# Kernel tuning notes

Hardware: AMD Instinct MI355X
Metric: run time of the kernel (lower is better)

Reference implementation:

```python
import jax, jax.numpy as jnp
import numpy as np

EMB_SCALE = 0.001  # embedding_scale when normalize=False


def setup_inputs() -> dict:
    key = jax.random.key(0)
    k1, k2 = jax.random.split(key)
    N, S, C, V, K = 8, 4096, 2, 128, 512
    x0 = jax.random.normal(k1, (N, S, C, V), dtype=jnp.float32)
    embedding = jax.random.normal(k2, (C, K, V), dtype=jnp.float32) * EMB_SCALE
    return {"x0": x0, "embedding": embedding}


def reference(x0, embedding):
    # normalize=False path: x = x0, embedding used as-is
    N, S, C, V = x0.shape
    K = embedding.shape[1]
    x = x0
    xf = x.reshape(N * S, C, V)  # (B, C, V), B = N*S tokens

    # (the ||x||^2 term is constant over k). Avoids materializing (B, C, K, V).
    dots = jnp.einsum('bcv,ckv->bck', xf, embedding)          # (B, C, K)
    e_sq = jnp.sum(embedding * embedding, axis=2)             # (C, K)
    dist2 = e_sq[None, :, :] - 2.0 * dots                     # (B, C, K)
    index = jnp.argmin(dist2, axis=2)                         # (B, C) int

    # Entropy of codebook usage (original divides by len(index) == B rows)
    B = N * S
    hist = jnp.bincount(index.reshape(-1), length=K).astype(jnp.float32)
    prob = hist / jnp.float32(B)
    entropy = -jnp.sum(jnp.where(hist > 0, prob * jnp.log(jnp.maximum(prob, 1e-30)), 0.0))

    # Gather: output[b, c] = embedding[c, index[b, c]]
    output = embedding[jnp.arange(C), index]                  # (B, C, V)
    output = output.reshape(N, S, C, V)

    out0 = jax.lax.stop_gradient(output - x) + x              # straight-through
    out1 = jnp.sum((jax.lax.stop_gradient(x) - output) ** 2, axis=3)  # (N,S,C)
    out2 = (jnp.sum((x - jax.lax.stop_gradient(output)) ** 2, axis=3)
            + jnp.sum((x - x0) ** 2, axis=3))                 # (N,S,C); (x-x0)==0 here
    return (out0, out1, out2, entropy)
```

## Files before the change

### kernel.cpp

```cpp
#include <hip/hip_runtime.h>
#include <math.h>

#define N_TOK    32768
#define C_CH     2
#define V_DIM    128
#define K_CODES  512
#define TPB      32
#define CAND_CAP 512
#define BAND     4.0e-3f

typedef short     bf16v8 __attribute__((ext_vector_type(8)));
typedef float     f32x4  __attribute__((ext_vector_type(4)));
typedef unsigned  u32x4  __attribute__((ext_vector_type(4)));
typedef __attribute__((address_space(1))) const unsigned char* gas_t;
typedef __attribute__((address_space(3))) unsigned char* las_t;

__device__ inline unsigned f2bf(float f) {
    unsigned u = __float_as_uint(f);
    return (u + 0x7FFFu + ((u >> 16) & 1u)) >> 16;
}
__device__ inline unsigned mapf(float d) {
    unsigned u = __float_as_uint(d);
    return ((int)u < 0) ? ~u : (u | 0x80000000u);
}
__device__ inline float unmapf(unsigned u) {
    return __uint_as_float((u & 0x80000000u) ? (u & 0x7FFFFFFFu) : ~u);
}

__global__ __launch_bounds__(64) void vq_prep(const float* __restrict__ emb,
                                              float* __restrict__ e_sq,
                                              unsigned int* __restrict__ hist,
                                              unsigned char* __restrict__ img) {
    const int row  = blockIdx.x;
    const int k    = row & (K_CODES - 1);
    const int lane = threadIdx.x;
    const float a = emb[(size_t)row * V_DIM + lane];
    const float b = emb[(size_t)row * V_DIM + 64 + lane];
    float s = a * a + b * b;
#pragma unroll
    for (int off = 32; off; off >>= 1) s += __shfl_down(s, off);
    if (lane == 0) {
        e_sq[row] = s;
        if (row < K_CODES) hist[row] = 0u;
    }
    if (lane < 16) {
        const int sp = lane;
        const int sl = sp ^ (k & 7);
        const float* src = emb + (size_t)row * V_DIM + sl * 8;
        u32x4 val;
#pragma unroll
        for (int q = 0; q < 4; ++q)
            val[q] = f2bf(src[2 * q]) | (f2bf(src[2 * q + 1]) << 16);
        *reinterpret_cast<u32x4*>(img + ((size_t)row * 16 + sp) * 16) = val;
    }
}

__global__ __launch_bounds__(256, 3) void vq_main(const float* __restrict__ x0,
                                                  const float* __restrict__ emb,
                                                  const float* __restrict__ e_sq,
                                                  const unsigned char* __restrict__ img,
                                                  unsigned int* __restrict__ hist,
                                                  float* __restrict__ out0,
                                                  float* __restrict__ out1,
                                                  float* __restrict__ out2) {
    __shared__ __align__(16) unsigned char es[128 * 256];
    __shared__ __align__(16) unsigned char xs[TPB * 256];
    __shared__ float xx_s[TPB];
    __shared__ unsigned int dmin_s[TPB];
    __shared__ unsigned long long best_s[TPB];
    __shared__ unsigned int cand[CAND_CAP];
    __shared__ int cand_n;

    const int c    = blockIdx.y;
    const int gt0  = blockIdx.x * TPB;
    const int t    = threadIdx.x;
    const int lane = t & 63;
    const int w    = t >> 6;
    const int l15  = lane & 15;
    const int l4   = lane >> 4;

    if (t < TPB) { dmin_s[t] = 0xFFFFFFFFu; best_s[t] = ~0ull; }
    if (t == 0) cand_n = 0;

    {
        const int row = t >> 3;
        const int q   = t & 7;
        const float* xp = x0 + ((size_t)(gt0 + row) * C_CH + c) * V_DIM + q * 16;
        f32x4 p0 = *reinterpret_cast<const f32x4*>(xp);
        f32x4 p1 = *reinterpret_cast<const f32x4*>(xp + 4);
        f32x4 p2 = *reinterpret_cast<const f32x4*>(xp + 8);
        f32x4 p3 = *reinterpret_cast<const f32x4*>(xp + 12);
        float part = 0.f;
#pragma unroll
        for (int z = 0; z < 4; ++z) {
            part = fmaf(p0[z], p0[z], part);
            part = fmaf(p1[z], p1[z], part);
            part = fmaf(p2[z], p2[z], part);
            part = fmaf(p3[z], p3[z], part);
        }
#pragma unroll
        for (int m2 = 1; m2 <= 4; m2 <<= 1) part += __shfl_xor(part, m2);
        if (q == 0) xx_s[row] = part;
        u32x4 v0, v1;
        v0[0] = f2bf(p0[0]) | (f2bf(p0[1]) << 16);
        v0[1] = f2bf(p0[2]) | (f2bf(p0[3]) << 16);
        v0[2] = f2bf(p1[0]) | (f2bf(p1[1]) << 16);
        v0[3] = f2bf(p1[2]) | (f2bf(p1[3]) << 16);
        v1[0] = f2bf(p2[0]) | (f2bf(p2[1]) << 16);
        v1[1] = f2bf(p2[2]) | (f2bf(p2[3]) << 16);
        v1[2] = f2bf(p3[0]) | (f2bf(p3[1]) << 16);
        v1[3] = f2bf(p3[2]) | (f2bf(p3[3]) << 16);
        const int s0 = (q * 2)     ^ (row & 7);
        const int s1 = (q * 2 + 1) ^ (row & 7);
        *reinterpret_cast<u32x4*>(xs + row * 256 + s0 * 16) = v0;
        *reinterpret_cast<u32x4*>(xs + row * 256 + s1 * 16) = v1;
    }

    float esq_r[8];
#pragma unroll
    for (int Q = 0; Q < 4; ++Q)
#pragma unroll
        for (int n = 0; n < 2; ++n)
            esq_r[Q * 2 + n] = e_sq[c * K_CODES + Q * 128 + w * 32 + n * 16 + l15];

    __syncthreads();

    u32x4 Af[2][4];
#pragma unroll
    for (int m = 0; m < 2; ++m)
#pragma unroll
        for (int kk = 0; kk < 4; ++kk) {
            const int row = m * 16 + l15;
            Af[m][kk] = *reinterpret_cast<const u32x4*>(
                xs + row * 256 + (((kk * 4 + l4) ^ (row & 7)) * 16));
        }

    float dt[2][8][4];
    const unsigned char* imgc = img + ((size_t)c * K_CODES) * 256;

#pragma unroll
    for (int Q = 0; Q < 4; ++Q) {
        __syncthreads();
        {
            const unsigned char* src = imgc + (size_t)Q * 128 * 256;
#pragma unroll
            for (int i = 0; i < 8; ++i) {
                const int off = (i * 4 + w) * 1024;
                __builtin_amdgcn_global_load_lds(
                    (gas_t)(src + off + lane * 16),
                    (las_t)(es + off), 16, 0, 0);
            }
        }
        __syncthreads();

#pragma unroll
        for (int n = 0; n < 2; ++n) {
            const int row = w * 32 + n * 16 + l15;
            u32x4 B[4];
#pragma unroll
            for (int kk = 0; kk < 4; ++kk)
                B[kk] = *reinterpret_cast<const u32x4*>(
                    es + row * 256 + (((kk * 4 + l4) ^ (row & 7)) * 16));
            f32x4 a0 = {0.f, 0.f, 0.f, 0.f};
            f32x4 a1 = {0.f, 0.f, 0.f, 0.f};
#pragma unroll
            for (int kk = 0; kk < 4; ++kk) {
                a0 = __builtin_amdgcn_mfma_f32_16x16x32_bf16(
                    __builtin_bit_cast(bf16v8, Af[0][kk]),
                    __builtin_bit_cast(bf16v8, B[kk]), a0, 0, 0, 0);
                a1 = __builtin_amdgcn_mfma_f32_16x16x32_bf16(
                    __builtin_bit_cast(bf16v8, Af[1][kk]),
                    __builtin_bit_cast(bf16v8, B[kk]), a1, 0, 0, 0);
            }
            const float esv = esq_r[Q * 2 + n];
#pragma unroll
            for (int r = 0; r < 4; ++r) {
                dt[0][Q * 2 + n][r] = fmaf(-2.f, a0[r], esv);
                dt[1][Q * 2 + n][r] = fmaf(-2.f, a1[r], esv);
            }
        }
    }

#pragma unroll
    for (int m = 0; m < 2; ++m)
#pragma unroll
        for (int r = 0; r < 4; ++r) {
            float v = dt[m][0][r];
#pragma unroll
            for (int qn = 1; qn < 8; ++qn) v = fminf(v, dt[m][qn][r]);
#pragma unroll
            for (int s = 1; s < 16; s <<= 1) v = fminf(v, __shfl_xor(v, s));
            if (l15 == 0) atomicMin(&dmin_s[m * 16 + l4 * 4 + r], mapf(v));
        }
    __syncthreads();

#pragma unroll
    for (int m = 0; m < 2; ++m)
#pragma unroll
        for (int r = 0; r < 4; ++r) {
            const int tok = m * 16 + l4 * 4 + r;
            const float thr = unmapf(dmin_s[tok]) + BAND;
#pragma unroll
            for (int qn = 0; qn < 8; ++qn) {
                if (dt[m][qn][r] <= thr) {
                    const int k = (qn >> 1) * 128 + w * 32 + (qn & 1) * 16 + l15;
                    const int pos = atomicAdd(&cand_n, 1);
                    if (pos < CAND_CAP)
                        cand[pos] = ((unsigned)tok << 9) | (unsigned)k;
                }
            }
        }
    __syncthreads();

    const int nc = cand_n < CAND_CAP ? cand_n : CAND_CAP;
    for (int i = t; i < nc; i += 256) {
        const unsigned key = cand[i];
        const int tok = key >> 9;
        const int kc  = key & (K_CODES - 1);
        const float* xg = x0 + ((size_t)(gt0 + tok) * C_CH + c) * V_DIM;
        const float* eg = emb + ((size_t)c * K_CODES + kc) * V_DIM;
        float a0 = 0.f, a1 = 0.f, a2 = 0.f, a3 = 0.f;
#pragma unroll 4
        for (int q = 0; q < 32; ++q) {
            const f32x4 xv = *reinterpret_cast<const f32x4*>(xg + q * 4);
            const f32x4 ev = *reinterpret_cast<const f32x4*>(eg + q * 4);
            a0 = fmaf(xv[0], ev[0], a0);
            a1 = fmaf(xv[1], ev[1], a1);
            a2 = fmaf(xv[2], ev[2], a2);
            a3 = fmaf(xv[3], ev[3], a3);
        }
        const float dot = (a0 + a1) + (a2 + a3);
        const float d   = fmaf(-2.f, dot, e_sq[c * K_CODES + kc]);
        atomicMin(&best_s[tok], ((unsigned long long)mapf(d) << 32) | (unsigned)kc);
    }
    __syncthreads();

    if (t < TPB) {
        const unsigned long long b = best_s[t];
        const int k = (int)(b & (unsigned)(K_CODES - 1));
        const float d = unmapf((unsigned)(b >> 32));
        const float o12 = xx_s[t] + d;
        const size_t oi = (size_t)(gt0 + t) * C_CH + c;
        out1[oi] = o12;
        out2[oi] = o12;
        atomicAdd(&hist[k], 1u);
    }

#pragma unroll
    for (int i = 0; i < 4; ++i) {
        const int tok = i * 8 + (t >> 5);
        const int v4  = t & 31;
        const int k   = (int)(best_s[tok] & (unsigned long long)(K_CODES - 1));
        const f32x4 ev = *reinterpret_cast<const f32x4*>(
            emb + ((size_t)c * K_CODES + k) * V_DIM + v4 * 4);
        const f32x4 xv = *reinterpret_cast<const f32x4*>(
            x0 + ((size_t)(gt0 + tok) * C_CH + c) * V_DIM + v4 * 4);
        f32x4 ov;
#pragma unroll
        for (int z = 0; z < 4; ++z) ov[z] = (ev[z] - xv[z]) + xv[z];
        *reinterpret_cast<f32x4*>(
            out0 + ((size_t)(gt0 + tok) * C_CH + c) * V_DIM + v4 * 4) = ov;
    }
}

__global__ __launch_bounds__(512) void vq_entropy(const unsigned int* __restrict__ hist,
                                                  float* __restrict__ ent) {
    const int t = threadIdx.x;
    float v = 0.f;
    const unsigned int h = hist[t];
    if (h > 0u) {
        const float p = (float)h * (1.0f / 32768.0f);
        v = p * logf(p);
    }
#pragma unroll
    for (int off = 32; off; off >>= 1) v += __shfl_down(v, off);
    __shared__ float s[8];
    if ((t & 63) == 0) s[t >> 6] = v;
    __syncthreads();
    if (t == 0) {
        float tot = 0.f;
#pragma unroll
        for (int i = 0; i < 8; ++i) tot += s[i];
        ent[0] = -tot;
    }
}

extern "C" void kernel_launch(void* const* d_in, const int* in_sizes, int n_in,
                              void* d_out, int out_size, void* d_ws, size_t ws_size,
                              hipStream_t stream) {
    const float* x0  = (const float*)d_in[0];
    const float* emb = (const float*)d_in[1];

    float*         e_sq = (float*)d_ws;
    unsigned int*  hist = (unsigned int*)((char*)d_ws + 4096);
    unsigned char* img  = (unsigned char*)d_ws + 8192;

    float* out0 = (float*)d_out;
    float* out1 = out0 + (size_t)N_TOK * C_CH * V_DIM;
    float* out2 = out1 + (size_t)N_TOK * C_CH;
    float* ent  = out2 + (size_t)N_TOK * C_CH;

    vq_prep<<<C_CH * K_CODES, 64, 0, stream>>>(emb, e_sq, hist, img);
    vq_main<<<dim3(N_TOK / TPB, C_CH), 256, 0, stream>>>(x0, emb, e_sq, img, hist,
                                                         out0, out1, out2);
    vq_entropy<<<1, K_CODES, 0, stream>>>(hist, ent);
}
```

Baseline: 74.45 us.

## Keep codebook slice in registers and stream token tiles through MFMA

Each wave now holds its 128-code slice of the bf16 codebook in registers for the whole block, instead of staging the codebook through shared memory in four passes. Each block handles 64 tokens, processed as four 16-token tiles, and the next tile's x0 rows are prefetched while the current tile runs. Candidate refinement now uses 16-lane groups with a shuffle reduction, and the histogram moves to a separate kernel fed by a 16-bit index buffer. The large register footprint lowers occupancy to 2 blocks per CU, and the extra launch adds overhead.

```diff
diff --git a/kernel.cpp b/kernel.cpp
--- a/kernel.cpp
+++ b/kernel.cpp
@@ -5,15 +5,13 @@
 #define C_CH     2
 #define V_DIM    128
 #define K_CODES  512
-#define TPB      32
-#define CAND_CAP 512
+#define TPB      64
+#define CAND_CAP 768
 #define BAND     4.0e-3f
 
 typedef short     bf16v8 __attribute__((ext_vector_type(8)));
 typedef float     f32x4  __attribute__((ext_vector_type(4)));
 typedef unsigned  u32x4  __attribute__((ext_vector_type(4)));
-typedef __attribute__((address_space(1))) const unsigned char* gas_t;
-typedef __attribute__((address_space(3))) unsigned char* las_t;
 
 __device__ inline unsigned f2bf(float f) {
     unsigned u = __float_as_uint(f);
@@ -32,7 +30,6 @@
                                               unsigned int* __restrict__ hist,
                                               unsigned char* __restrict__ img) {
     const int row  = blockIdx.x;
-    const int k    = row & (K_CODES - 1);
     const int lane = threadIdx.x;
     const float a = emb[(size_t)row * V_DIM + lane];
     const float b = emb[(size_t)row * V_DIM + 64 + lane];
@@ -44,27 +41,23 @@
         if (row < K_CODES) hist[row] = 0u;
     }
     if (lane < 16) {
-        const int sp = lane;
-        const int sl = sp ^ (k & 7);
-        const float* src = emb + (size_t)row * V_DIM + sl * 8;
+        const float* src = emb + (size_t)row * V_DIM + lane * 8;
         u32x4 val;
 #pragma unroll
         for (int q = 0; q < 4; ++q)
             val[q] = f2bf(src[2 * q]) | (f2bf(src[2 * q + 1]) << 16);
-        *reinterpret_cast<u32x4*>(img + ((size_t)row * 16 + sp) * 16) = val;
-    }
-}
-
-__global__ __launch_bounds__(256, 3) void vq_main(const float* __restrict__ x0,
+        *reinterpret_cast<u32x4*>(img + ((size_t)row * 16 + lane) * 16) = val;
+    }
+}
+
+__global__ __launch_bounds__(256, 2) void vq_main(const float* __restrict__ x0,
                                                   const float* __restrict__ emb,
                                                   const float* __restrict__ e_sq,
                                                   const unsigned char* __restrict__ img,
-                                                  unsigned int* __restrict__ hist,
+                                                  unsigned short* __restrict__ idx16,
                                                   float* __restrict__ out0,
                                                   float* __restrict__ out1,
                                                   float* __restrict__ out2) {
-    __shared__ __align__(16) unsigned char es[128 * 256];
-    __shared__ __align__(16) unsigned char xs[TPB * 256];
     __shared__ float xx_s[TPB];
     __shared__ unsigned int dmin_s[TPB];
     __shared__ unsigned long long best_s[TPB];
@@ -82,156 +75,133 @@
     if (t < TPB) { dmin_s[t] = 0xFFFFFFFFu; best_s[t] = ~0ull; }
     if (t == 0) cand_n = 0;
 
+    u32x4 Bf[8][4];
     {
-        const int row = t >> 3;
-        const int q   = t & 7;
-        const float* xp = x0 + ((size_t)(gt0 + row) * C_CH + c) * V_DIM + q * 16;
-        f32x4 p0 = *reinterpret_cast<const f32x4*>(xp);
-        f32x4 p1 = *reinterpret_cast<const f32x4*>(xp + 4);
-        f32x4 p2 = *reinterpret_cast<const f32x4*>(xp + 8);
-        f32x4 p3 = *reinterpret_cast<const f32x4*>(xp + 12);
+        const unsigned char* imgc = img + (size_t)(c * K_CODES + w * 128) * 256;
+#pragma unroll
+        for (int ct = 0; ct < 8; ++ct)
+#pragma unroll
+            for (int kk = 0; kk < 4; ++kk)
+                Bf[ct][kk] = *reinterpret_cast<const u32x4*>(
+                    imgc + (size_t)(ct * 16 + l15) * 256 + (kk * 4 + l4) * 16);
+    }
+    float esq_r[8];
+#pragma unroll
+    for (int ct = 0; ct < 8; ++ct)
+        esq_r[ct] = e_sq[c * K_CODES + w * 128 + ct * 16 + l15];
+
+    __syncthreads();
+
+    f32x4 raw[8];
+    auto LOADX = [&](int tile_) {
+        const float* xp = x0 + ((size_t)(gt0 + tile_ * 16 + l15) * C_CH + c) * V_DIM
+                        + l4 * 8;
+#pragma unroll
+        for (int kk = 0; kk < 4; ++kk) {
+            raw[2 * kk]     = *reinterpret_cast<const f32x4*>(xp + kk * 32);
+            raw[2 * kk + 1] = *reinterpret_cast<const f32x4*>(xp + kk * 32 + 4);
+        }
+    };
+
+    LOADX(0);
+#pragma unroll
+    for (int tile = 0; tile < 4; ++tile) {
+        u32x4 A[4];
         float part = 0.f;
 #pragma unroll
-        for (int z = 0; z < 4; ++z) {
-            part = fmaf(p0[z], p0[z], part);
-            part = fmaf(p1[z], p1[z], part);
-            part = fmaf(p2[z], p2[z], part);
-            part = fmaf(p3[z], p3[z], part);
-        }
-#pragma unroll
-        for (int m2 = 1; m2 <= 4; m2 <<= 1) part += __shfl_xor(part, m2);
-        if (q == 0) xx_s[row] = part;
-        u32x4 v0, v1;
-        v0[0] = f2bf(p0[0]) | (f2bf(p0[1]) << 16);
-        v0[1] = f2bf(p0[2]) | (f2bf(p0[3]) << 16);
-        v0[2] = f2bf(p1[0]) | (f2bf(p1[1]) << 16);
-        v0[3] = f2bf(p1[2]) | (f2bf(p1[3]) << 16);
-        v1[0] = f2bf(p2[0]) | (f2bf(p2[1]) << 16);
-        v1[1] = f2bf(p2[2]) | (f2bf(p2[3]) << 16);
-        v1[2] = f2bf(p3[0]) | (f2bf(p3[1]) << 16);
-        v1[3] = f2bf(p3[2]) | (f2bf(p3[3]) << 16);
-        const int s0 = (q * 2)     ^ (row & 7);
-        const int s1 = (q * 2 + 1) ^ (row & 7);
-        *reinterpret_cast<u32x4*>(xs + row * 256 + s0 * 16) = v0;
-        *reinterpret_cast<u32x4*>(xs + row * 256 + s1 * 16) = v1;
-    }
-
-    float esq_r[8];
-#pragma unroll
-    for (int Q = 0; Q < 4; ++Q)
-#pragma unroll
-        for (int n = 0; n < 2; ++n)
-            esq_r[Q * 2 + n] = e_sq[c * K_CODES + Q * 128 + w * 32 + n * 16 + l15];
-
-    __syncthreads();
-
-    u32x4 Af[2][4];
-#pragma unroll
-    for (int m = 0; m < 2; ++m)
-#pragma unroll
         for (int kk = 0; kk < 4; ++kk) {
-            const int row = m * 16 + l15;
-            Af[m][kk] = *reinterpret_cast<const u32x4*>(
-                xs + row * 256 + (((kk * 4 + l4) ^ (row & 7)) * 16));
-        }
-
-    float dt[2][8][4];
-    const unsigned char* imgc = img + ((size_t)c * K_CODES) * 256;
-
-#pragma unroll
-    for (int Q = 0; Q < 4; ++Q) {
+            const f32x4 lo = raw[2 * kk], hi = raw[2 * kk + 1];
+            u32x4 v;
+            v[0] = f2bf(lo[0]) | (f2bf(lo[1]) << 16);
+            v[1] = f2bf(lo[2]) | (f2bf(lo[3]) << 16);
+            v[2] = f2bf(hi[0]) | (f2bf(hi[1]) << 16);
+            v[3] = f2bf(hi[2]) | (f2bf(hi[3]) << 16);
+            A[kk] = v;
+#pragma unroll
+            for (int z = 0; z < 4; ++z) {
+                part = fmaf(lo[z], lo[z], part);
+                part = fmaf(hi[z], hi[z], part);
+            }
+        }
+        part += __shfl_xor(part, 16);
+        part += __shfl_xor(part, 32);
+        if (w == 0 && l4 == 0) xx_s[tile * 16 + l15] = part;
+
+        if (tile < 3) LOADX(tile + 1);
+
+        f32x4 acc[8];
+#pragma unroll
+        for (int ct = 0; ct < 8; ++ct) acc[ct] = (f32x4){0.f, 0.f, 0.f, 0.f};
+#pragma unroll
+        for (int kk = 0; kk < 4; ++kk)
+#pragma unroll
+            for (int ct = 0; ct < 8; ++ct)
+                acc[ct] = __builtin_amdgcn_mfma_f32_16x16x32_bf16(
+                    __builtin_bit_cast(bf16v8, A[kk]),
+                    __builtin_bit_cast(bf16v8, Bf[ct][kk]), acc[ct], 0, 0, 0);
+
+#pragma unroll
+        for (int ct = 0; ct < 8; ++ct)
+#pragma unroll
+            for (int r = 0; r < 4; ++r)
+                acc[ct][r] = fmaf(-2.f, acc[ct][r], esq_r[ct]);
+#pragma unroll
+        for (int r = 0; r < 4; ++r) {
+            float v = acc[0][r];
+#pragma unroll
+            for (int ct = 1; ct < 8; ++ct) v = fminf(v, acc[ct][r]);
+#pragma unroll
+            for (int s = 1; s < 16; s <<= 1) v = fminf(v, __shfl_xor(v, s));
+            if (l15 == 0)
+                atomicMin(&dmin_s[tile * 16 + l4 * 4 + r], mapf(v));
+        }
         __syncthreads();
-        {
-            const unsigned char* src = imgc + (size_t)Q * 128 * 256;
-#pragma unroll
-            for (int i = 0; i < 8; ++i) {
-                const int off = (i * 4 + w) * 1024;
-                __builtin_amdgcn_global_load_lds(
-                    (gas_t)(src + off + lane * 16),
-                    (las_t)(es + off), 16, 0, 0);
-            }
-        }
-        __syncthreads();
-
-#pragma unroll
-        for (int n = 0; n < 2; ++n) {
-            const int row = w * 32 + n * 16 + l15;
-            u32x4 B[4];
-#pragma unroll
-            for (int kk = 0; kk < 4; ++kk)
-                B[kk] = *reinterpret_cast<const u32x4*>(
-                    es + row * 256 + (((kk * 4 + l4) ^ (row & 7)) * 16));
-            f32x4 a0 = {0.f, 0.f, 0.f, 0.f};
-            f32x4 a1 = {0.f, 0.f, 0.f, 0.f};
-#pragma unroll
-            for (int kk = 0; kk < 4; ++kk) {
-                a0 = __builtin_amdgcn_mfma_f32_16x16x32_bf16(
-                    __builtin_bit_cast(bf16v8, Af[0][kk]),
-                    __builtin_bit_cast(bf16v8, B[kk]), a0, 0, 0, 0);
-                a1 = __builtin_amdgcn_mfma_f32_16x16x32_bf16(
-                    __builtin_bit_cast(bf16v8, Af[1][kk]),
-                    __builtin_bit_cast(bf16v8, B[kk]), a1, 0, 0, 0);
-            }
-            const float esv = esq_r[Q * 2 + n];
-#pragma unroll
-            for (int r = 0; r < 4; ++r) {
-                dt[0][Q * 2 + n][r] = fmaf(-2.f, a0[r], esv);
-                dt[1][Q * 2 + n][r] = fmaf(-2.f, a1[r], esv);
-            }
-        }
-    }
-
-#pragma unroll
-    for (int m = 0; m < 2; ++m)
+
 #pragma unroll
         for (int r = 0; r < 4; ++r) {
-            float v = dt[m][0][r];
-#pragma unroll
-            for (int qn = 1; qn < 8; ++qn) v = fminf(v, dt[m][qn][r]);
-#pragma unroll
-            for (int s = 1; s < 16; s <<= 1) v = fminf(v, __shfl_xor(v, s));
-            if (l15 == 0) atomicMin(&dmin_s[m * 16 + l4 * 4 + r], mapf(v));
-        }
-    __syncthreads();
-
-#pragma unroll
-    for (int m = 0; m < 2; ++m)
-#pragma unroll
-        for (int r = 0; r < 4; ++r) {
-            const int tok = m * 16 + l4 * 4 + r;
+            const int tok = tile * 16 + l4 * 4 + r;
             const float thr = unmapf(dmin_s[tok]) + BAND;
 #pragma unroll
-            for (int qn = 0; qn < 8; ++qn) {
-                if (dt[m][qn][r] <= thr) {
-                    const int k = (qn >> 1) * 128 + w * 32 + (qn & 1) * 16 + l15;
+            for (int ct = 0; ct < 8; ++ct) {
+                if (acc[ct][r] <= thr) {
+                    const int k = w * 128 + ct * 16 + l15;
                     const int pos = atomicAdd(&cand_n, 1);
                     if (pos < CAND_CAP)
                         cand[pos] = ((unsigned)tok << 9) | (unsigned)k;
                 }
             }
         }
-    __syncthreads();
-
-    const int nc = cand_n < CAND_CAP ? cand_n : CAND_CAP;
-    for (int i = t; i < nc; i += 256) {
-        const unsigned key = cand[i];
-        const int tok = key >> 9;
-        const int kc  = key & (K_CODES - 1);
-        const float* xg = x0 + ((size_t)(gt0 + tok) * C_CH + c) * V_DIM;
-        const float* eg = emb + ((size_t)c * K_CODES + kc) * V_DIM;
-        float a0 = 0.f, a1 = 0.f, a2 = 0.f, a3 = 0.f;
-#pragma unroll 4
-        for (int q = 0; q < 32; ++q) {
-            const f32x4 xv = *reinterpret_cast<const f32x4*>(xg + q * 4);
-            const f32x4 ev = *reinterpret_cast<const f32x4*>(eg + q * 4);
-            a0 = fmaf(xv[0], ev[0], a0);
-            a1 = fmaf(xv[1], ev[1], a1);
-            a2 = fmaf(xv[2], ev[2], a2);
-            a3 = fmaf(xv[3], ev[3], a3);
-        }
-        const float dot = (a0 + a1) + (a2 + a3);
-        const float d   = fmaf(-2.f, dot, e_sq[c * K_CODES + kc]);
-        atomicMin(&best_s[tok], ((unsigned long long)mapf(d) << 32) | (unsigned)kc);
+    }
+    __syncthreads();
+
+    {
+        const int nc = cand_n < CAND_CAP ? cand_n : CAND_CAP;
+        const int g  = t >> 4;
+        const int gl = t & 15;
+        for (int i = g; i < nc; i += 16) {
+            const unsigned key = cand[i];
+            const int tok = key >> 9;
+            const int kc  = key & (K_CODES - 1);
+            const float* xg = x0 + ((size_t)(gt0 + tok) * C_CH + c) * V_DIM + gl * 8;
+            const float* eg = emb + ((size_t)c * K_CODES + kc) * V_DIM + gl * 8;
+            const f32x4 xa = *reinterpret_cast<const f32x4*>(xg);
+            const f32x4 xb = *reinterpret_cast<const f32x4*>(xg + 4);
+            const f32x4 ea = *reinterpret_cast<const f32x4*>(eg);
+            const f32x4 eb = *reinterpret_cast<const f32x4*>(eg + 4);
+            float d8 = 0.f;
+#pragma unroll
+            for (int z = 0; z < 4; ++z) {
+                d8 = fmaf(xa[z], ea[z], d8);
+                d8 = fmaf(xb[z], eb[z], d8);
+            }
+#pragma unroll
+            for (int s = 1; s < 16; s <<= 1) d8 += __shfl_xor(d8, s);
+            if (gl == 0) {
+                const float d = fmaf(-2.f, d8, e_sq[c * K_CODES + kc]);
+                atomicMin(&best_s[tok],
+                          ((unsigned long long)mapf(d) << 32) | (unsigned)kc);
+            }
+        }
     }
     __syncthreads();
 
@@ -243,12 +213,12 @@
         const size_t oi = (size_t)(gt0 + t) * C_CH + c;
         out1[oi] = o12;
         out2[oi] = o12;
-        atomicAdd(&hist[k], 1u);
-    }
-
-#pragma unroll
-    for (int i = 0; i < 4; ++i) {
-        const int tok = i * 8 + (t >> 5);
+        idx16[oi] = (unsigned short)k;
+    }
+
+#pragma unroll
+    for (int p = 0; p < 8; ++p) {
+        const int tok = p * 8 + (t >> 5);
         const int v4  = t & 31;
         const int k   = (int)(best_s[tok] & (unsigned long long)(K_CODES - 1));
         const f32x4 ev = *reinterpret_cast<const f32x4*>(
@@ -261,6 +231,21 @@
         *reinterpret_cast<f32x4*>(
             out0 + ((size_t)(gt0 + tok) * C_CH + c) * V_DIM + v4 * 4) = ov;
     }
+}
+
+__global__ __launch_bounds__(256) void vq_hist(const unsigned short* __restrict__ idx16,
+                                               unsigned int* __restrict__ hist) {
+    __shared__ unsigned int h[K_CODES];
+    const int t = threadIdx.x;
+    h[t] = 0u; h[t + 256] = 0u;
+    __syncthreads();
+    const int base = blockIdx.x * 4096;
+#pragma unroll
+    for (int j = 0; j < 16; ++j)
+        atomicAdd(&h[idx16[base + j * 256 + t]], 1u);
+    __syncthreads();
+    if (h[t])       atomicAdd(&hist[t],       h[t]);
+    if (h[t + 256]) atomicAdd(&hist[t + 256], h[t + 256]);
 }
 
 __global__ __launch_bounds__(512) void vq_entropy(const unsigned int* __restrict__ hist,
@@ -291,9 +276,10 @@
     const float* x0  = (const float*)d_in[0];
     const float* emb = (const float*)d_in[1];
 
-    float*         e_sq = (float*)d_ws;
-    unsigned int*  hist = (unsigned int*)((char*)d_ws + 4096);
-    unsigned char* img  = (unsigned char*)d_ws + 8192;
+    float*          e_sq  = (float*)d_ws;
+    unsigned int*   hist  = (unsigned int*)((char*)d_ws + 4096);
+    unsigned char*  img   = (unsigned char*)d_ws + 8192;
+    unsigned short* idx16 = (unsigned short*)((char*)d_ws + 8192 + 262144);
 
     float* out0 = (float*)d_out;
     float* out1 = out0 + (size_t)N_TOK * C_CH * V_DIM;
@@ -301,7 +287,8 @@
     float* ent  = out2 + (size_t)N_TOK * C_CH;
 
     vq_prep<<<C_CH * K_CODES, 64, 0, stream>>>(emb, e_sq, hist, img);
-    vq_main<<<dim3(N_TOK / TPB, C_CH), 256, 0, stream>>>(x0, emb, e_sq, img, hist,
+    vq_main<<<dim3(N_TOK / TPB, C_CH), 256, 0, stream>>>(x0, emb, e_sq, img, idx16,
                                                          out0, out1, out2);
+    vq_hist<<<16, 256, 0, stream>>>(idx16, hist);
     vq_entropy<<<1, K_CODES, 0, stream>>>(hist, ent);
 }
```

Result: slower. 76.64 us (+2.9%).
